# Kernel tuning notes

Measured on AMD Instinct MI355X. Metric: run time of the kernel, lower is better.

Reference implementation:

```python
import jax, jax.numpy as jnp
import numpy as np

B, S, D = 4, 1024, 1024
H, DK, DV = 16, 64, 64


def setup_inputs() -> dict:
    key = jax.random.key(0)
    ks = jax.random.split(key, 8)
    sc = 0.02
    return {
        "queries": jax.random.normal(ks[0], (B, S, D), jnp.float32),
        "keys": jax.random.normal(ks[1], (B, S, D), jnp.float32),
        "values": jax.random.normal(ks[2], (B, S, D), jnp.float32),
        "attn_bias": jax.random.normal(ks[3], (B, 1, S, S), jnp.float32),
        "Wq": jax.random.normal(ks[4], (H * DK, D), jnp.float32) * sc,
        "Wk": jax.random.normal(ks[5], (H * DK, D), jnp.float32) * sc,
        "Wv": jax.random.normal(ks[6], (H * DV, D), jnp.float32) * sc,
        "Wp": jax.random.normal(ks[7], (D, H * DV), jnp.float32) * sc,
    }


def reference(queries, keys, values, attn_bias, Wq, Wk, Wv, Wp):
    # Linear (no bias): x @ W.T, then split heads -> [B, H, S, d]
    q = (queries @ Wq.T).reshape(B, S, H, DK).transpose(0, 2, 1, 3)
    k = (keys @ Wk.T).reshape(B, S, H, DK).transpose(0, 2, 1, 3)
    v = (values @ Wv.T).reshape(B, S, H, DV).transpose(0, 2, 1, 3)
    # NOTE: original scales by d_model**-0.5, not d_key**-0.5
    scores = jnp.einsum("bhqd,bhkd->bhqk", q, k) * (D ** -0.5)
    scores = scores + attn_bias  # bias broadcasts over heads
    weights = jax.nn.softmax(scores, axis=-1)
    out = jnp.einsum("bhqk,bhkd->bhqd", weights, v)  # [B,H,S,DV]
    out = out.transpose(0, 2, 1, 3).reshape(B, S, H * DV)
    return out @ Wp.T
```

## Files before the change

### kernel.cpp

```cpp
#include <hip/hip_runtime.h>
#include <hip/hip_bf16.h>

typedef unsigned short u16;
typedef unsigned int u32;
typedef __attribute__((ext_vector_type(8))) short bf16x8;
typedef __attribute__((ext_vector_type(8))) u16 u16x8;
typedef __attribute__((ext_vector_type(4))) u16 u16x4;
typedef __attribute__((ext_vector_type(4))) u32 u32x4;
typedef __attribute__((ext_vector_type(4))) float f32x4;
typedef __attribute__((ext_vector_type(16))) float f32x16;

typedef const __attribute__((address_space(1))) void* gas1_t;
typedef __attribute__((address_space(3))) void* las3_t;

#define MFMA16(a,b,c) __builtin_amdgcn_mfma_f32_16x16x32_bf16((a),(b),(c),0,0,0)
#define MFMA32(a,b,c) __builtin_amdgcn_mfma_f32_32x32x16_bf16((a),(b),(c),0,0,0)

static constexpr int BB = 4, SS = 1024, DD = 1024, HH = 16;

static __device__ __forceinline__ u16 f2b(float x) {
  union { __hip_bfloat16 h; u16 u; } cv;
  cv.h = __float2bfloat16(x);
  return cv.u;
}
static __device__ __forceinline__ u32 pk2(float a, float b) {
  return (u32)f2b(a) | ((u32)f2b(b) << 16);
}

__global__ __launch_bounds__(256) void cvt_all(
    const float* __restrict__ q, const float* __restrict__ k, const float* __restrict__ v,
    const float* __restrict__ wq_, const float* __restrict__ wk_, const float* __restrict__ wv_,
    const float* __restrict__ wp_,
    u16* __restrict__ qb, u16* __restrict__ kb, u16* __restrict__ vb,
    u16* __restrict__ wqb, u16* __restrict__ wkb, u16* __restrict__ wvb, u16* __restrict__ wpb) {
  int bid = blockIdx.x;
  const float* s; u16* d; int off;
  if      (bid < 4096)  { s = q;   d = qb;  off = bid; }
  else if (bid < 8192)  { s = k;   d = kb;  off = bid - 4096; }
  else if (bid < 12288) { s = v;   d = vb;  off = bid - 8192; }
  else if (bid < 13312) { s = wq_; d = wqb; off = bid - 12288; }
  else if (bid < 14336) { s = wk_; d = wkb; off = bid - 13312; }
  else if (bid < 15360) { s = wv_; d = wvb; off = bid - 14336; }
  else                  { s = wp_; d = wpb; off = bid - 15360; }
  int i = (off * 256 + threadIdx.x) * 4;
  float4 val = *(const float4*)(s + i);
  u16x4 r = { f2b(val.x), f2b(val.y), f2b(val.z), f2b(val.w) };
  *(u16x4*)(d + i) = r;
}

template<typename OT>
__global__ __launch_bounds__(256) void gemm_bt(
    const u16* __restrict__ Abase, const u16* __restrict__ Wbase, OT* __restrict__ Cbase,
    int N, int K, size_t sA, size_t sW, size_t sC) {
  const u16* A = Abase + (size_t)blockIdx.z * sA;
  const u16* W = Wbase + (size_t)blockIdx.z * sW;
  OT* C = Cbase + (size_t)blockIdx.z * sC;

  __shared__ __align__(16) u16 As[128 * 32];
  __shared__ __align__(16) u16 Bs[128 * 32];

  const int tid = threadIdx.x;
  const int lane = tid & 63;
  const int wid = tid >> 6;
  const int g = lane >> 4;
  const int li = lane & 15;
  const int brow = blockIdx.y * 128;
  const int bcol = blockIdx.x * 128;
  const int wr = (wid >> 1) * 64;
  const int wc = (wid & 1) * 64;

  const int srow = tid >> 2;
  const int scol = (tid & 3) * 8;

  f32x4 acc[4][4] = {};

  for (int k0 = 0; k0 < K; k0 += 32) {
#pragma unroll
    for (int c = 0; c < 2; ++c) {
      const u16* ga = A + (size_t)(brow + srow + c * 64) * K + k0 + scol;
      const u16* gw = W + (size_t)(bcol + srow + c * 64) * K + k0 + scol;
      __builtin_amdgcn_global_load_lds((gas1_t)(const void*)ga,
                                       (las3_t)(void*)(As + wid * 512 + c * 2048), 16, 0, 0);
      __builtin_amdgcn_global_load_lds((gas1_t)(const void*)gw,
                                       (las3_t)(void*)(Bs + wid * 512 + c * 2048), 16, 0, 0);
    }
    __syncthreads();

    bf16x8 a[4], b[4];
#pragma unroll
    for (int m = 0; m < 4; ++m)
      a[m] = *(const bf16x8*)&As[(wr + m * 16 + li) * 32 + g * 8];
#pragma unroll
    for (int n = 0; n < 4; ++n)
      b[n] = *(const bf16x8*)&Bs[(wc + n * 16 + li) * 32 + g * 8];
#pragma unroll
    for (int m = 0; m < 4; ++m)
#pragma unroll
      for (int n = 0; n < 4; ++n)
        acc[m][n] = MFMA16(a[m], b[n], acc[m][n]);
    __syncthreads();
  }

#pragma unroll
  for (int m = 0; m < 4; ++m)
#pragma unroll
    for (int n = 0; n < 4; ++n)
#pragma unroll
      for (int j = 0; j < 4; ++j) {
        int r = brow + wr + m * 16 + g * 4 + j;
        int c = bcol + wc + n * 16 + li;
        if constexpr (sizeof(OT) == 2) C[(size_t)r * N + c] = (OT)f2b(acc[m][n][j]);
        else                           C[(size_t)r * N + c] = acc[m][n][j];
      }
}

__global__ __launch_bounds__(256) void transpose_v(const u16* __restrict__ V, u16* __restrict__ Vt) {
  __shared__ __align__(16) u16 t[64][72];
  const int s0 = blockIdx.x * 64, h = blockIdx.y, b = blockIdx.z;
  const int tid = threadIdx.x;
#pragma unroll
  for (int it = 0; it < 2; ++it) {
    int slot = tid + it * 256;
    int r = slot >> 3, seg = slot & 7;
    *(u16x8*)&t[r][seg * 8] = *(const u16x8*)&V[(size_t)(b * SS + s0 + r) * DD + h * 64 + seg * 8];
  }
  __syncthreads();
#pragma unroll
  for (int it = 0; it < 2; ++it) {
    int slot = tid + it * 256;
    int dv = slot >> 3, seg = slot & 7;
    u16x8 v;
#pragma unroll
    for (int i = 0; i < 8; ++i) v[i] = t[seg * 8 + i][dv];
    *(u16x8*)&Vt[(size_t)((b * HH + h) * 64 + dv) * SS + s0 + seg * 8] = v;
  }
}

__global__ __launch_bounds__(256) void attn_kernel(
    const u16* __restrict__ Q, const u16* __restrict__ K, const u16* __restrict__ Vt,
    const float* __restrict__ bias, u16* __restrict__ O) {
  __shared__ __align__(16) u16 kbuf[2][64 * 64];
  __shared__ __align__(16) u16 vbuf[2][64 * 64];
  __shared__ __align__(16) float bbuf[8192];

  const int tid = threadIdx.x;
  const int lane = tid & 63;
  const int wq = tid >> 6;
  const int hi = lane >> 5;
  const int ln = lane & 31;
  const u32 swz = (u32)(ln & 7) << 4;

  const int flat = blockIdx.x + (blockIdx.y << 3) + (blockIdx.z << 7);
  const int L = ((flat & 7) << 6) | (flat >> 3);
  const int qt = L & 7, h = (L >> 3) & 15, b = L >> 7;
  const int q0 = qt * 128;
  const int qrow = q0 + wq * 32 + ln;

  bf16x8 qf[4];
  {
    const u16* qp = Q + (size_t)(b * SS + qrow) * DD + h * 64 + hi * 8;
#pragma unroll
    for (int d = 0; d < 4; ++d) qf[d] = *(const bf16x8*)(qp + d * 16);
  }

  const int sr = tid >> 2;
  const int scb = (tid & 3) * 32;
  const u16* kg = K + (size_t)(b * SS + sr) * DD + h * 64 + scb / 2;
  const u16* vg = Vt + (size_t)((b * HH + h) * 64 + sr) * SS + scb / 2;
  const u32 wa0 = (u32)sr * 128 + (((u32)scb) ^ ((u32)(sr & 7) << 4));
  const u32 wa1 = (u32)sr * 128 + (((u32)scb + 16) ^ ((u32)(sr & 7) << 4));

  const int brow_ = tid >> 4;
  const int bgl = (tid & 15) ^ (brow_ & 15);
  const float* bsrc = bias + (size_t)(b * SS + q0 + brow_) * SS + bgl * 4;
  char* bdst = (char*)bbuf + wq * 1024;

  const int qq = wq * 32 + ln;
  const char* bb_base = (const char*)bbuf + qq * 256;
  int baddr[2][4];
#pragma unroll
  for (int kb = 0; kb < 2; ++kb)
#pragma unroll
    for (int rq = 0; rq < 4; ++rq)
      baddr[kb][rq] = ((kb * 8 + rq * 2 + hi) ^ (qq & 15)) << 4;

  u16x8 kr0, kr1, vr0, vr1;
  kr0 = *(const u16x8*)(kg + 0);
  kr1 = *(const u16x8*)(kg + 8);
  vr0 = *(const u16x8*)(vg + 0);
  vr1 = *(const u16x8*)(vg + 8);
  *(u16x8*)((char*)kbuf[0] + wa0) = kr0;
  *(u16x8*)((char*)kbuf[0] + wa1) = kr1;
  *(u16x8*)((char*)vbuf[0] + wa0) = vr0;
  *(u16x8*)((char*)vbuf[0] + wa1) = vr1;
  __syncthreads();

  f32x16 o0 = {}, o1 = {};
  float m = -1e30f, lsum = 0.f;
  int cur = 0;

  for (int kt = 0; kt < 16; ++kt) {
    {
      const float* bs = bsrc + kt * 64;
#pragma unroll
      for (int i = 0; i < 8; ++i)
        __builtin_amdgcn_global_load_lds((gas1_t)(const void*)(bs + i * 16384),
                                         (las3_t)(void*)(bdst + i * 4096), 16, 0, 0);
    }
    if (kt < 15) {
      const size_t k1 = (size_t)(kt + 1) * 64;
      kr0 = *(const u16x8*)(kg + k1 * DD + 0);
      kr1 = *(const u16x8*)(kg + k1 * DD + 8);
      vr0 = *(const u16x8*)(vg + k1 + 0);
      vr1 = *(const u16x8*)(vg + k1 + 8);
    }

    const char* kb_base = (const char*)kbuf[cur];
    f32x16 s[2];
#pragma unroll
    for (int kb = 0; kb < 2; ++kb) {
      f32x16 acc = {};
#pragma unroll
      for (int d = 0; d < 4; ++d) {
        bf16x8 kf = *(const bf16x8*)(kb_base + (kb * 32 + ln) * 128 + (((u32)(d * 32 + hi * 16)) ^ swz));
        acc = MFMA32(kf, qf[d], acc);
      }
      s[kb] = acc;
    }

    __syncthreads();

#pragma unroll
    for (int kb = 0; kb < 2; ++kb)
#pragma unroll
      for (int rq = 0; rq < 4; ++rq) {
        f32x4 bbv = *(const f32x4*)(bb_base + baddr[kb][rq]);
#pragma unroll
        for (int c = 0; c < 4; ++c)
          s[kb][rq * 4 + c] = fmaf(s[kb][rq * 4 + c], 0.03125f, bbv[c]);
      }

    float mt = -1e30f;
#pragma unroll
    for (int r = 0; r < 16; ++r) { mt = fmaxf(mt, s[0][r]); mt = fmaxf(mt, s[1][r]); }
    mt = fmaxf(mt, __shfl_xor(mt, 32));

    bool resc = false;
    float fsc = 1.f;
    if (kt == 0) {
      m = mt;
    } else if (__any(mt > m + 8.f)) {
      float mn = fmaxf(m, mt);
      fsc = __expf(m - mn);
      m = mn;
      resc = true;
    }

    float rs = 0.f;
    u32 wv[2][8];
#pragma unroll
    for (int kb = 0; kb < 2; ++kb)
#pragma unroll
      for (int t = 0; t < 8; ++t) {
        float p0 = __expf(s[kb][2 * t] - m);
        float p1 = __expf(s[kb][2 * t + 1] - m);
        rs += p0 + p1;
        wv[kb][t] = pk2(p0, p1);
      }
    rs += __shfl_xor(rs, 32);
    lsum = lsum * fsc + rs;

    if (resc) {
#pragma unroll
      for (int j = 0; j < 16; ++j) {
        float fv = __shfl(fsc, (j & 3) + 8 * (j >> 2) + 4 * hi);
        o0[j] *= fv; o1[j] *= fv;
      }
    }

    const char* vb_base = (const char*)vbuf[cur];
#pragma unroll
    for (int ks = 0; ks < 4; ++ks) {
      const int kb = ks >> 1, i0 = (ks & 1) * 4;
      u32 sA = hi ? wv[kb][i0 + 0] : wv[kb][i0 + 2];
      u32 sB = hi ? wv[kb][i0 + 1] : wv[kb][i0 + 3];
      u32 rA = (u32)__shfl_xor((int)sA, 32);
      u32 rB = (u32)__shfl_xor((int)sB, 32);
      u32 e0 = hi ? rA : wv[kb][i0 + 0];
      u32 e1 = hi ? rB : wv[kb][i0 + 1];
      u32 e2 = hi ? wv[kb][i0 + 2] : rA;
      u32 e3 = hi ? wv[kb][i0 + 3] : rB;
      union { u32x4 u; bf16x8 v; } pc;
      pc.u = (u32x4){e0, e1, e2, e3};
      bf16x8 pa = pc.v;
#pragma unroll
      for (int nv = 0; nv < 2; ++nv) {
        bf16x8 vf = *(const bf16x8*)(vb_base + (nv * 32 + ln) * 128 + (((u32)(ks * 32 + hi * 16)) ^ swz));
        if (nv == 0) o0 = MFMA32(pa, vf, o0);
        else         o1 = MFMA32(pa, vf, o1);
      }
    }

    if (kt < 15) {
      char* kd = (char*)kbuf[cur ^ 1];
      char* vd = (char*)vbuf[cur ^ 1];
      *(u16x8*)(kd + wa0) = kr0;
      *(u16x8*)(kd + wa1) = kr1;
      *(u16x8*)(vd + wa0) = vr0;
      *(u16x8*)(vd + wa1) = vr1;
    }
    __syncthreads();
    cur ^= 1;
  }

  float inv = 1.0f / lsum;
#pragma unroll
  for (int j = 0; j < 16; ++j) {
    float iv = __shfl(inv, (j & 3) + 8 * (j >> 2) + 4 * hi);
    int q = q0 + wq * 32 + (j & 3) + 8 * (j >> 2) + 4 * hi;
    u16* op = O + (size_t)(b * SS + q) * DD + h * 64 + ln;
    op[0]  = f2b(o0[j] * iv);
    op[32] = f2b(o1[j] * iv);
  }
}

extern "C" void kernel_launch(void* const* d_in, const int* in_sizes, int n_in,
                              void* d_out, int out_size, void* d_ws, size_t ws_size,
                              hipStream_t stream) {
  const float* queries = (const float*)d_in[0];
  const float* keys    = (const float*)d_in[1];
  const float* values  = (const float*)d_in[2];
  const float* bias    = (const float*)d_in[3];
  const float* Wq      = (const float*)d_in[4];
  const float* Wk      = (const float*)d_in[5];
  const float* Wv      = (const float*)d_in[6];
  const float* Wp      = (const float*)d_in[7];
  float* out = (float*)d_out;

  char* ws = (char*)d_ws;
  const size_t MB = 1024 * 1024;
  u16* qb  = (u16*)(ws + 0 * MB);
  u16* kb  = (u16*)(ws + 8 * MB);
  u16* vb  = (u16*)(ws + 16 * MB);
  u16* wqb = (u16*)(ws + 24 * MB);
  u16* wkb = (u16*)(ws + 26 * MB);
  u16* wvb = (u16*)(ws + 28 * MB);
  u16* wpb = (u16*)(ws + 30 * MB);
  u16* Qb  = (u16*)(ws + 32 * MB);
  u16* Kb  = (u16*)(ws + 40 * MB);
  u16* Vb  = (u16*)(ws + 48 * MB);
  u16* Vtb = (u16*)(ws + 56 * MB);
  u16* Ob  = (u16*)(ws + 0 * MB);

  const int nAct = BB * SS * DD;
  const int nW = DD * DD;

  cvt_all<<<dim3(16384), dim3(256), 0, stream>>>(
      queries, keys, values, Wq, Wk, Wv, Wp,
      qb, kb, vb, wqb, wkb, wvb, wpb);

  gemm_bt<u16><<<dim3(8, 32, 3), dim3(256), 0, stream>>>(
      qb, wqb, Qb, DD, DD, (size_t)nAct, (size_t)nW, (size_t)nAct);

  transpose_v<<<dim3(16, 16, 4), dim3(256), 0, stream>>>(Vb, Vtb);

  attn_kernel<<<dim3(8, 16, 4), dim3(256), 0, stream>>>(Qb, Kb, Vtb, bias, Ob);

  gemm_bt<float><<<dim3(8, 32, 1), dim3(256), 0, stream>>>(
      Ob, wpb, out, DD, DD, 0, 0, 0);
}
```

Measured before the change: 134.5 us.

## Pre-convert attention bias to fp16 and double-buffer bias tiles in LDS

A new kernel converts the fp32 attention bias to fp16 before attention runs. The attention kernel now reads half as many bias bytes per tile, and each bias tile is reused across 16 heads. Bias tiles are double-buffered in LDS and prefetched one iteration ahead, so the mid-loop __syncthreads that used to guard the single bias buffer is removed. The cost is an extra launch that streams the full fp32 bias once, plus the accuracy loss of rounding the bias to fp16.

```diff
diff --git a/kernel.cpp b/kernel.cpp
--- a/kernel.cpp
+++ b/kernel.cpp
@@ -8,6 +8,7 @@
 typedef __attribute__((ext_vector_type(4))) u16 u16x4;
 typedef __attribute__((ext_vector_type(4))) u32 u32x4;
 typedef __attribute__((ext_vector_type(4))) float f32x4;
+typedef __attribute__((ext_vector_type(4))) _Float16 f16x4;
 typedef __attribute__((ext_vector_type(16))) float f32x16;
 
 typedef const __attribute__((address_space(1))) void* gas1_t;
@@ -48,6 +49,14 @@
   *(u16x4*)(d + i) = r;
 }
 
+__global__ __launch_bounds__(256) void cvt_bias(const float* __restrict__ src,
+                                                _Float16* __restrict__ dst) {
+  int i = (blockIdx.x * 256 + threadIdx.x) * 4;
+  float4 v = *(const float4*)(src + i);
+  f16x4 r = { (_Float16)v.x, (_Float16)v.y, (_Float16)v.z, (_Float16)v.w };
+  *(f16x4*)(dst + i) = r;
+}
+
 template<typename OT>
 __global__ __launch_bounds__(256) void gemm_bt(
     const u16* __restrict__ Abase, const u16* __restrict__ Wbase, OT* __restrict__ Cbase,
@@ -138,10 +147,10 @@
 
 __global__ __launch_bounds__(256) void attn_kernel(
     const u16* __restrict__ Q, const u16* __restrict__ K, const u16* __restrict__ Vt,
-    const float* __restrict__ bias, u16* __restrict__ O) {
+    const _Float16* __restrict__ bias16, u16* __restrict__ O) {
   __shared__ __align__(16) u16 kbuf[2][64 * 64];
   __shared__ __align__(16) u16 vbuf[2][64 * 64];
-  __shared__ __align__(16) float bbuf[8192];
+  __shared__ __align__(16) u16 bbuf[2][8192];
 
   const int tid = threadIdx.x;
   const int lane = tid & 63;
@@ -170,20 +179,25 @@
   const u32 wa0 = (u32)sr * 128 + (((u32)scb) ^ ((u32)(sr & 7) << 4));
   const u32 wa1 = (u32)sr * 128 + (((u32)scb + 16) ^ ((u32)(sr & 7) << 4));
 
-  const int brow_ = tid >> 4;
-  const int bgl = (tid & 15) ^ (brow_ & 15);
-  const float* bsrc = bias + (size_t)(b * SS + q0 + brow_) * SS + bgl * 4;
-  char* bdst = (char*)bbuf + wq * 1024;
+  const int r_l = lane >> 3;
+  const int gl = (lane & 7) ^ r_l;
+  const _Float16* bsrc = bias16 + (size_t)(b * SS + q0 + wq * 8 + r_l) * SS + gl * 8;
 
   const int qq = wq * 32 + ln;
-  const char* bb_base = (const char*)bbuf + qq * 256;
   int baddr[2][4];
 #pragma unroll
   for (int kb = 0; kb < 2; ++kb)
 #pragma unroll
     for (int rq = 0; rq < 4; ++rq)
-      baddr[kb][rq] = ((kb * 8 + rq * 2 + hi) ^ (qq & 15)) << 4;
-
+      baddr[kb][rq] = qq * 128 + (((kb * 4 + rq) ^ (ln & 7)) << 4) + hi * 8;
+
+  {
+    char* bd = (char*)bbuf[0] + wq * 1024;
+#pragma unroll
+    for (int i = 0; i < 4; ++i)
+      __builtin_amdgcn_global_load_lds((gas1_t)(const void*)(bsrc + (size_t)i * 32 * SS),
+                                       (las3_t)(void*)(bd + i * 4096), 16, 0, 0);
+  }
   u16x8 kr0, kr1, vr0, vr1;
   kr0 = *(const u16x8*)(kg + 0);
   kr1 = *(const u16x8*)(kg + 8);
@@ -200,14 +214,13 @@
   int cur = 0;
 
   for (int kt = 0; kt < 16; ++kt) {
-    {
-      const float* bs = bsrc + kt * 64;
-#pragma unroll
-      for (int i = 0; i < 8; ++i)
-        __builtin_amdgcn_global_load_lds((gas1_t)(const void*)(bs + i * 16384),
-                                         (las3_t)(void*)(bdst + i * 4096), 16, 0, 0);
-    }
     if (kt < 15) {
+      char* bd = (char*)bbuf[cur ^ 1] + wq * 1024;
+      const _Float16* bs = bsrc + (kt + 1) * 64;
+#pragma unroll
+      for (int i = 0; i < 4; ++i)
+        __builtin_amdgcn_global_load_lds((gas1_t)(const void*)(bs + (size_t)i * 32 * SS),
+                                         (las3_t)(void*)(bd + i * 4096), 16, 0, 0);
       const size_t k1 = (size_t)(kt + 1) * 64;
       kr0 = *(const u16x8*)(kg + k1 * DD + 0);
       kr1 = *(const u16x8*)(kg + k1 * DD + 8);
@@ -228,16 +241,15 @@
       s[kb] = acc;
     }
 
-    __syncthreads();
-
+    const char* bbr = (const char*)bbuf[cur];
 #pragma unroll
     for (int kb = 0; kb < 2; ++kb)
 #pragma unroll
       for (int rq = 0; rq < 4; ++rq) {
-        f32x4 bbv = *(const f32x4*)(bb_base + baddr[kb][rq]);
+        f16x4 bv = *(const f16x4*)(bbr + baddr[kb][rq]);
 #pragma unroll
         for (int c = 0; c < 4; ++c)
-          s[kb][rq * 4 + c] = fmaf(s[kb][rq * 4 + c], 0.03125f, bbv[c]);
+          s[kb][rq * 4 + c] = fmaf(s[kb][rq * 4 + c], 0.03125f, (float)bv[c]);
       }
 
     float mt = -1e30f;
@@ -308,9 +320,9 @@
       *(u16x8*)(kd + wa1) = kr1;
       *(u16x8*)(vd + wa0) = vr0;
       *(u16x8*)(vd + wa1) = vr1;
-    }
-    __syncthreads();
-    cur ^= 1;
+      __syncthreads();
+      cur ^= 1;
+    }
   }
 
   float inv = 1.0f / lsum;
@@ -350,6 +362,7 @@
   u16* Kb  = (u16*)(ws + 40 * MB);
   u16* Vb  = (u16*)(ws + 48 * MB);
   u16* Vtb = (u16*)(ws + 56 * MB);
+  _Float16* bias16 = (_Float16*)(ws + 8 * MB);
   u16* Ob  = (u16*)(ws + 0 * MB);
 
   const int nAct = BB * SS * DD;
@@ -364,7 +377,9 @@
 
   transpose_v<<<dim3(16, 16, 4), dim3(256), 0, stream>>>(Vb, Vtb);
 
-  attn_kernel<<<dim3(8, 16, 4), dim3(256), 0, stream>>>(Qb, Kb, Vtb, bias, Ob);
+  cvt_bias<<<dim3(4096), dim3(256), 0, stream>>>(bias, bias16);
+
+  attn_kernel<<<dim3(8, 16, 4), dim3(256), 0, stream>>>(Qb, Kb, Vtb, bias16, Ob);
 
   gemm_bt<float><<<dim3(8, 32, 1), dim3(256), 0, stream>>>(
       Ob, wpb, out, DD, DD, 0, 0, 0);
```

New measurement: 138.2 us. +2.7%, slower.
